# Kernel optimization log

Hardware: AMD Instinct MI355X
Metric: run time of the kernel (lower is better)

Reference implementation:

```python
import jax, jax.numpy as jnp
from jax import lax
import numpy as np

H, W, C = 2160, 3840, 3
CROP = 3  # rows trimmed top and bottom before filtering


def median1d(x, size, axis):
    """Sliding-window median along `axis` with edge padding (matches
    np.pad(mode='edge') + centered window + np.median for odd size)."""
    pad = size // 2
    pw = [(0, 0)] * x.ndim
    pw[axis] = (pad, pad)
    xp = jnp.pad(x, pw, mode='edge')
    n = x.shape[axis]
    # stack the `size` shifted views -> (..., size), median = middle of sort
    windows = jnp.stack(
        [lax.slice_in_dim(xp, i, i + n, axis=axis) for i in range(size)], axis=-1)
    return jnp.sort(windows, axis=-1)[..., size // 2]


def shift1(x, axis):
    """np.pad(x,(1,0),'constant')[:-1] along `axis`: shift forward, zero-fill."""
    pw = [(0, 0)] * x.ndim
    pw[axis] = (1, 0)
    return lax.slice_in_dim(jnp.pad(x, pw), 0, x.shape[axis], axis=axis)


def setup_inputs() -> dict:
    key = jax.random.key(0)
    k1, k2 = jax.random.split(key)
    img = jax.random.normal(k1, (H, W, C), dtype=jnp.float32)
    mask = jax.random.randint(k2, (H, W), 0, 2, dtype=jnp.int32)
    return {"img": img, "mask": mask, "vertical_size": 5}


def reference(img, mask, vertical_size):
    # mask is read but unused by the original module's math.
    x = img[CROP:-CROP]                       # (H-6, W, C)
    # vertical pass: median(v), shift down 1, median(3) along rows
    v = median1d(x, vertical_size, axis=0)
    v = median1d(shift1(v, axis=0), 3, axis=0)
    # horizontal pass (original reuses vertical_size here): along columns
    h = median1d(v, vertical_size, axis=1)
    h = median1d(shift1(h, axis=1), 3, axis=1)
    return h
```

## Files before the change

### kernel.cpp

```cpp
#include <hip/hip_runtime.h>

#define HH    2160
#define WW    3840
#define CROPC 3
#define NN    (HH - 2*CROPC)
#define WFLAT (WW * 3)

constexpr int TY    = 16;
constexpr int OPW   = 46;
constexpr int WPB   = 4;
constexpr int NTH   = 64 * WPB;
constexpr int OPB   = OPW * WPB;
constexpr int XROWS = TY + 6;

__device__ __forceinline__ float vmed3(float a, float b, float c) {
    float r;
    asm("v_med3_f32 %0, %1, %2, %3" : "=v"(r) : "v"(a), "v"(b), "v"(c));
    return r;
}
__device__ __forceinline__ float med5_7(float a, float b, float c, float d, float e) {
    const float lo1 = fminf(a, b), hi1 = fmaxf(a, b);
    const float lo2 = fminf(c, d), hi2 = fmaxf(c, d);
    return vmed3(e, fmaxf(lo1, lo2), fminf(hi1, hi2));
}

__global__ __launch_bounds__(NTH, 8) void fused_median(const float* __restrict__ img,
                                                       float* __restrict__ out) {
    const int tid  = threadIdx.x;
    const int lane = tid & 63;
    const int wv   = tid >> 6;
    const int r0   = blockIdx.y * TY;
    const int fp12 = blockIdx.x * OPB + wv * OPW + lane;
    const int fl   = fp12 - 12;
    const int ch   = fp12 % 3;
    const int cc   = min(max(fp12 / 3 - 4, 0), WW - 1);
    const float* colp = img + (size_t)CROPC * WFLAT + (cc * 3 + ch);

    const int  ci       = fl / 3;
    const bool store_ok = (lane >= 12) && (lane < 58) && (fl < WFLAT);

    const int lm6 = max(lane - 6, 0), lm3 = max(lane - 3, 0);
    const int lp3 = min(lane + 3, 63), lp6 = min(lane + 6, 63);

    float xv[XROWS];
    #pragma unroll
    for (int i = 0; i < XROWS; ++i) {
        const int rr = min(max(r0 - 4 + i, 0), NN - 1);
        xv[i] = colp[(size_t)rr * WFLAT];
    }
    asm volatile("" ::
        "v"(xv[0]),  "v"(xv[1]),  "v"(xv[2]),  "v"(xv[3]),  "v"(xv[4]),
        "v"(xv[5]),  "v"(xv[6]),  "v"(xv[7]),  "v"(xv[8]),  "v"(xv[9]),
        "v"(xv[10]), "v"(xv[11]), "v"(xv[12]), "v"(xv[13]), "v"(xv[14]),
        "v"(xv[15]), "v"(xv[16]), "v"(xv[17]), "v"(xv[18]), "v"(xv[19]),
        "v"(xv[20]), "v"(xv[21]));

    float lo0 = fminf(xv[0], xv[1]), hi0 = fmaxf(xv[0], xv[1]);
    float lo1 = fminf(xv[1], xv[2]), hi1 = fmaxf(xv[1], xv[2]);
    float vm2 = 0.f, vm1 = 0.f;
    #pragma unroll
    for (int s = 0; s < TY + 2; ++s) {
        const float lo2 = fminf(xv[s+2], xv[s+3]);
        const float hi2 = fmaxf(xv[s+2], xv[s+3]);
        const float vc  = vmed3(xv[s+4], fmaxf(lo0, lo2), fminf(hi0, hi2));
        if (s >= 2) {
            const int rz = r0 + s - 2;
            float a = vm2, b = vm1;
            if (rz == NN - 1) a = b;
            if (rz == 1)      a = 0.f;
            if (rz == 0)    { a = 0.f; b = 0.f; }
            const float w = vmed3(a, b, vc);

            const float m6 = __shfl(w, lm6, 64);
            const float m3 = __shfl(w, lm3, 64);
            const float p3 = __shfl(w, lp3, 64);
            const float p6 = __shfl(w, lp6, 64);
            const float h0 = med5_7(m6, m3, p3, p6, w);

            const float hm3 = __shfl(h0, lm3, 64);
            const float hm6 = __shfl(h0, lm6, 64);
            float A = hm6, B = hm3;
            if (ci == WW - 1) A = B;
            if (ci == 1)      A = 0.f;
            if (ci == 0)    { A = 0.f; B = 0.f; }
            const float o = vmed3(A, B, h0);

            if (store_ok && rz < NN)
                out[(size_t)rz * WFLAT + fl] = o;
        }
        lo0 = lo1; hi0 = hi1; lo1 = lo2; hi1 = hi2;
        vm2 = vm1; vm1 = vc;
    }
}

extern "C" void kernel_launch(void* const* d_in, const int* in_sizes, int n_in,
                              void* d_out, int out_size, void* d_ws, size_t ws_size,
                              hipStream_t stream) {
    const float* img = (const float*)d_in[0];
    float* out = (float*)d_out;
    dim3 grid((WFLAT + OPB - 1) / OPB,
              (NN + TY - 1) / TY);
    fused_median<<<grid, NTH, 0, stream>>>(img, out);
}
```

Baseline: 48.78 us.

## Process two adjacent flat elements per lane with float2 loads and stores

Each lane now handles two consecutive flattened pixel-channel elements, loading them as float2 (with a scalar fallback at clamped edges) and storing float2 results. The horizontal shuffle pattern is rewritten for the pair layout, so each wave covers 110 outputs instead of 46. This cuts the halo overhead per wave and halves the number of memory instructions. The cost is more registers per thread, and occupancy drops to 6 waves per SIMD. The float2 stores also need an even fl0, which holds because OPW is even.

```diff
diff --git a/kernel.cpp b/kernel.cpp
--- a/kernel.cpp
+++ b/kernel.cpp
@@ -7,7 +7,7 @@
 #define WFLAT (WW * 3)
 
 constexpr int TY    = 16;
-constexpr int OPW   = 46;
+constexpr int OPW   = 110;
 constexpr int WPB   = 4;
 constexpr int NTH   = 64 * WPB;
 constexpr int OPB   = OPW * WPB;
@@ -19,77 +19,100 @@
     return r;
 }
 __device__ __forceinline__ float med5_7(float a, float b, float c, float d, float e) {
-    const float lo1 = fminf(a, b), hi1 = fmaxf(a, b);
-    const float lo2 = fminf(c, d), hi2 = fmaxf(c, d);
-    return vmed3(e, fmaxf(lo1, lo2), fminf(hi1, hi2));
+    return vmed3(e, fmaxf(fminf(a, b), fminf(c, d)), fminf(fmaxf(a, b), fmaxf(c, d)));
 }
 
-__global__ __launch_bounds__(NTH, 8) void fused_median(const float* __restrict__ img,
+__global__ __launch_bounds__(NTH, 6) void fused_median(const float* __restrict__ img,
                                                        float* __restrict__ out) {
     const int tid  = threadIdx.x;
     const int lane = tid & 63;
     const int wv   = tid >> 6;
     const int r0   = blockIdx.y * TY;
-    const int fp12 = blockIdx.x * OPB + wv * OPW + lane;
-    const int fl   = fp12 - 12;
-    const int ch   = fp12 % 3;
-    const int cc   = min(max(fp12 / 3 - 4, 0), WW - 1);
-    const float* colp = img + (size_t)CROPC * WFLAT + (cc * 3 + ch);
+    const int fp12 = blockIdx.x * OPB + wv * OPW + 2 * lane;
+    const int fl0  = fp12 - 12;
 
-    const int  ci       = fl / 3;
-    const bool store_ok = (lane >= 12) && (lane < 58) && (fl < WFLAT);
+    const int ch0  = fp12 % 3,       ch1  = (fp12 + 1) % 3;
+    const int ci0  = fp12 / 3 - 4,   ci1  = (fp12 + 1) / 3 - 4;
+    const int a0   = min(max(ci0, 0), WW - 1) * 3 + ch0;
+    const int a1   = min(max(ci1, 0), WW - 1) * 3 + ch1;
+    const bool contig = (a1 == a0 + 1);
+    const float* base = img + (size_t)CROPC * WFLAT;
 
-    const int lm6 = max(lane - 6, 0), lm3 = max(lane - 3, 0);
-    const int lp3 = min(lane + 3, 63), lp6 = min(lane + 6, 63);
+    const bool store_ok = (lane >= 6) && (lane <= 60) && (fl0 < WFLAT);
 
-    float xv[XROWS];
-    #pragma unroll
-    for (int i = 0; i < XROWS; ++i) {
-        const int rr = min(max(r0 - 4 + i, 0), NN - 1);
-        xv[i] = colp[(size_t)rr * WFLAT];
+    const int sm1 = max(lane - 1, 0), sm2 = max(lane - 2, 0), sm3 = max(lane - 3, 0);
+    const int sp1 = min(lane + 1, 63), sp2 = min(lane + 2, 63), sp3 = min(lane + 3, 63);
+
+    float2 xv[XROWS];
+    if (contig) {
+        #pragma unroll
+        for (int i = 0; i < XROWS; ++i) {
+            const int rr = min(max(r0 - 4 + i, 0), NN - 1);
+            xv[i] = *(const float2*)(base + (size_t)rr * WFLAT + a0);
+        }
+    } else {
+        #pragma unroll
+        for (int i = 0; i < XROWS; ++i) {
+            const int rr = min(max(r0 - 4 + i, 0), NN - 1);
+            const float* rp = base + (size_t)rr * WFLAT;
+            xv[i] = make_float2(rp[a0], rp[a1]);
+        }
     }
     asm volatile("" ::
-        "v"(xv[0]),  "v"(xv[1]),  "v"(xv[2]),  "v"(xv[3]),  "v"(xv[4]),
-        "v"(xv[5]),  "v"(xv[6]),  "v"(xv[7]),  "v"(xv[8]),  "v"(xv[9]),
-        "v"(xv[10]), "v"(xv[11]), "v"(xv[12]), "v"(xv[13]), "v"(xv[14]),
-        "v"(xv[15]), "v"(xv[16]), "v"(xv[17]), "v"(xv[18]), "v"(xv[19]),
-        "v"(xv[20]), "v"(xv[21]));
+        "v"(xv[0].x),"v"(xv[0].y),"v"(xv[1].x),"v"(xv[1].y),"v"(xv[2].x),"v"(xv[2].y),
+        "v"(xv[3].x),"v"(xv[3].y),"v"(xv[4].x),"v"(xv[4].y),"v"(xv[5].x),"v"(xv[5].y),
+        "v"(xv[6].x),"v"(xv[6].y),"v"(xv[7].x),"v"(xv[7].y));
+    asm volatile("" ::
+        "v"(xv[8].x),"v"(xv[8].y),"v"(xv[9].x),"v"(xv[9].y),"v"(xv[10].x),"v"(xv[10].y),
+        "v"(xv[11].x),"v"(xv[11].y),"v"(xv[12].x),"v"(xv[12].y),"v"(xv[13].x),"v"(xv[13].y),
+        "v"(xv[14].x),"v"(xv[14].y));
+    asm volatile("" ::
+        "v"(xv[15].x),"v"(xv[15].y),"v"(xv[16].x),"v"(xv[16].y),"v"(xv[17].x),"v"(xv[17].y),
+        "v"(xv[18].x),"v"(xv[18].y),"v"(xv[19].x),"v"(xv[19].y),"v"(xv[20].x),"v"(xv[20].y),
+        "v"(xv[21].x),"v"(xv[21].y));
 
-    float lo0 = fminf(xv[0], xv[1]), hi0 = fmaxf(xv[0], xv[1]);
-    float lo1 = fminf(xv[1], xv[2]), hi1 = fmaxf(xv[1], xv[2]);
-    float vm2 = 0.f, vm1 = 0.f;
+    float lo0x = fminf(xv[0].x, xv[1].x), hi0x = fmaxf(xv[0].x, xv[1].x);
+    float lo1x = fminf(xv[1].x, xv[2].x), hi1x = fmaxf(xv[1].x, xv[2].x);
+    float lo0y = fminf(xv[0].y, xv[1].y), hi0y = fmaxf(xv[0].y, xv[1].y);
+    float lo1y = fminf(xv[1].y, xv[2].y), hi1y = fmaxf(xv[1].y, xv[2].y);
+    float vm2x = 0.f, vm1x = 0.f, vm2y = 0.f, vm1y = 0.f;
+
     #pragma unroll
     for (int s = 0; s < TY + 2; ++s) {
-        const float lo2 = fminf(xv[s+2], xv[s+3]);
-        const float hi2 = fmaxf(xv[s+2], xv[s+3]);
-        const float vc  = vmed3(xv[s+4], fmaxf(lo0, lo2), fminf(hi0, hi2));
+        const float lo2x = fminf(xv[s+2].x, xv[s+3].x), hi2x = fmaxf(xv[s+2].x, xv[s+3].x);
+        const float lo2y = fminf(xv[s+2].y, xv[s+3].y), hi2y = fmaxf(xv[s+2].y, xv[s+3].y);
+        const float vcx = vmed3(xv[s+4].x, fmaxf(lo0x, lo2x), fminf(hi0x, hi2x));
+        const float vcy = vmed3(xv[s+4].y, fmaxf(lo0y, lo2y), fminf(hi0y, hi2y));
         if (s >= 2) {
             const int rz = r0 + s - 2;
-            float a = vm2, b = vm1;
-            if (rz == NN - 1) a = b;
-            if (rz == 1)      a = 0.f;
-            if (rz == 0)    { a = 0.f; b = 0.f; }
-            const float w = vmed3(a, b, vc);
+            float ax = vm2x, bx = vm1x, ay = vm2y, by = vm1y;
+            if (rz == NN - 1) { ax = bx; ay = by; }
+            if (rz == 1)      { ax = 0.f; ay = 0.f; }
+            if (rz == 0)      { ax = 0.f; bx = 0.f; ay = 0.f; by = 0.f; }
+            const float wx = vmed3(ax, bx, vcx);
+            const float wy = vmed3(ay, by, vcy);
 
-            const float m6 = __shfl(w, lm6, 64);
-            const float m3 = __shfl(w, lm3, 64);
-            const float p3 = __shfl(w, lp3, 64);
-            const float p6 = __shfl(w, lp6, 64);
-            const float h0 = med5_7(m6, m3, p3, p6, w);
+            const float h0 = med5_7(__shfl(wx, sm3, 64), __shfl(wy, sm2, 64),
+                                    __shfl(wy, sp1, 64), __shfl(wx, sp3, 64), wx);
+            const float h1v = med5_7(__shfl(wy, sm3, 64), __shfl(wx, sm1, 64),
+                                     __shfl(wx, sp2, 64), __shfl(wy, sp3, 64), wy);
 
-            const float hm3 = __shfl(h0, lm3, 64);
-            const float hm6 = __shfl(h0, lm6, 64);
-            float A = hm6, B = hm3;
-            if (ci == WW - 1) A = B;
-            if (ci == 1)      A = 0.f;
-            if (ci == 0)    { A = 0.f; B = 0.f; }
-            const float o = vmed3(A, B, h0);
+            float A = __shfl(h0, sm3, 64), B = __shfl(h1v, sm2, 64);
+            if (ci0 == WW - 1) A = B;
+            if (ci0 == 1)      A = 0.f;
+            if (ci0 == 0)    { A = 0.f; B = 0.f; }
+            const float o0 = vmed3(A, B, h0);
+            float C = __shfl(h1v, sm3, 64), D = __shfl(h0, sm1, 64);
+            if (ci1 == WW - 1) C = D;
+            if (ci1 == 1)      C = 0.f;
+            if (ci1 == 0)    { C = 0.f; D = 0.f; }
+            const float o1 = vmed3(C, D, h1v);
 
             if (store_ok && rz < NN)
-                out[(size_t)rz * WFLAT + fl] = o;
+                *(float2*)(out + (size_t)rz * WFLAT + fl0) = make_float2(o0, o1);
         }
-        lo0 = lo1; hi0 = hi1; lo1 = lo2; hi1 = hi2;
-        vm2 = vm1; vm1 = vc;
+        lo0x = lo1x; hi0x = hi1x; lo1x = lo2x; hi1x = hi2x; vm2x = vm1x; vm1x = vcx;
+        lo0y = lo1y; hi0y = hi1y; lo1y = lo2y; hi1y = hi2y; vm2y = vm1y; vm1y = vcy;
     }
 }
 
```

Measured after the change: 71.17 us. +45.9%, slower.
